# Kernel optimization log

Measured on AMD Instinct MI355X. Metric: run time of the kernel, lower is better.

The kernel has to match this reference:

```python
import jax, jax.numpy as jnp
import numpy as np
from jax import lax

RANK = 8
ALPHA = 16.0
SCALING = ALPHA / RANK  # 2.0
C_IN, C_OUT, KH, KW = 128, 256, 3, 3


def setup_inputs() -> dict:
    key = jax.random.key(0)
    k1, k2, k3, k4, k5 = jax.random.split(key, 5)
    x = jax.random.normal(k1, (16, C_IN, 64, 64), dtype=jnp.float32)
    W = jax.random.normal(k2, (C_OUT, C_IN, KH, KW), dtype=jnp.float32) * 0.05
    b = jax.random.normal(k3, (C_OUT,), dtype=jnp.float32) * 0.05
    lora_A = jax.random.normal(k4, (RANK, C_IN * KH * KW), dtype=jnp.float32) * 0.02
    lora_B = jax.random.normal(k5, (C_OUT, RANK), dtype=jnp.float32) * 0.02
    return {"x": x, "W": W, "b": b, "lora_A": lora_A, "lora_B": lora_B}


def _conv(x, w, stride=(1, 1), padding=((1, 1), (1, 1))):
    return lax.conv_general_dilated(
        x, w, window_strides=stride, padding=padding,
        dimension_numbers=("NCHW", "OIHW", "NCHW"))


def reference(x, W, b, lora_A, lora_B):
    # Base (frozen) conv: [B, C_out, H, W]
    base_out = _conv(x, W) + b[None, :, None, None]
    # LoRA path. The torch code does im2col -> (BL, C_in*kh*kw) @ A.T @ B.T.
    # Because unfold flattens patches channel-major as (C_in, kh, kw), the
    # identical math is: rank-r conv with A reshaped as [rank, C_in, kh, kw],
    # then a 1x1 mix with B. Same result, no im2col materialization.
    A_k = lora_A.reshape(RANK, C_IN, KH, KW)
    h = _conv(x, A_k)                                   # [B, rank, H, W]
    lora_out = jnp.einsum("brhw,or->bohw", h, lora_B) * SCALING
    return base_out + lora_out
```

## Files before the change

kernel.cpp:

```cpp
#include <hip/hip_runtime.h>
#include <hip/hip_bf16.h>


#define CIN   128
#define COUT  256
#define NBAT  16
#define HPAD  66
#define WPAD  66

typedef __bf16 bf16x8 __attribute__((ext_vector_type(8)));
typedef float f32x4 __attribute__((ext_vector_type(4)));

#define XPAD_ELEMS ((size_t)NBAT * HPAD * WPAD * CIN)
#define XPAD_BYTES (XPAD_ELEMS * 2)
#define WT_ELEMS   ((size_t)9 * COUT * CIN)
#define WS_NEED    (XPAD_BYTES + WT_ELEMS * 2)

typedef __attribute__((address_space(1))) void gvoid;
typedef __attribute__((address_space(3))) void lvoid;

__device__ __forceinline__ void load_lds16(const void* g, void* l) {
    __builtin_amdgcn_global_load_lds((gvoid*)g, (lvoid*)l, 16, 0, 0);
}

__global__ void pad_prep(const float* __restrict__ x, __bf16* __restrict__ xpad,
                         const float* __restrict__ W, const float* __restrict__ lA,
                         const float* __restrict__ lB, __hip_bfloat16* __restrict__ Wt) {
    __shared__ float tile[128][66];
    const int t = threadIdx.x;

    if (blockIdx.x >= 1024) {
        const int idx = (blockIdx.x - 1024) * 256 + t;
        const int c = idx & 127;
        const int o = idx >> 7;
        float lb[8];
#pragma unroll
        for (int r = 0; r < 8; ++r) lb[r] = lB[o * 8 + r];
#pragma unroll
        for (int tap = 0; tap < 9; ++tap) {
            float acc = W[(o * 128 + c) * 9 + tap];
            float s = 0.f;
#pragma unroll
            for (int r = 0; r < 8; ++r)
                s += lb[r] * lA[r * 1152 + c * 9 + tap];
            Wt[tap * 32768 + idx] = __float2bfloat16(acc + 2.0f * s);
        }
        return;
    }

    const int n = blockIdx.x >> 6;
    const int h = blockIdx.x & 63;
    const float* src = x + (size_t)n * 128 * 4096 + (size_t)h * 64;
#pragma unroll
    for (int i = 0; i < 8; ++i) {
        int g  = i * 256 + t;
        int c  = g >> 4;
        int w4 = (g & 15) * 4;
        const float4 v = *reinterpret_cast<const float4*>(src + (size_t)c * 4096 + w4);
        const int wb = w4 ^ (((c >> 3) & 7) << 2);
        tile[c][wb + 0] = v.x; tile[c][wb + 1] = v.y;
        tile[c][wb + 2] = v.z; tile[c][wb + 3] = v.w;
    }
    __syncthreads();
    __bf16* dst = xpad + ((size_t)(n * 66 + h + 1) * 66 + 1) * 128;
#pragma unroll
    for (int i = 0; i < 4; ++i) {
        int g  = i * 256 + t;
        int w  = g >> 4;
        int c0 = (g & 15) * 8;
        const int swr = ((c0 >> 3) & 7) << 2;
        bf16x8 v;
#pragma unroll
        for (int j = 0; j < 8; ++j) v[j] = (__bf16)tile[c0 + j][w ^ swr];
        *reinterpret_cast<bf16x8*>(dst + (size_t)w * 128 + c0) = v;
    }
    bf16x8 z = {};
    __bf16* rowbase = xpad + (size_t)(n * 66 + h + 1) * 66 * 128;
    if (t < 32) {
        int ww = (t < 16) ? 0 : 65;
        int c0 = (t & 15) * 8;
        *reinterpret_cast<bf16x8*>(rowbase + (size_t)ww * 128 + c0) = z;
    }
    if (h == 0 || h == 63) {
        __bf16* hrow = xpad + (size_t)(n * 66 + (h == 0 ? 0 : 65)) * 66 * 128;
        for (int i = t; i < 66 * 16; i += 256)
            *reinterpret_cast<bf16x8*>(hrow + (size_t)i * 8) = z;
    }
}

__global__ void __launch_bounds__(512, 2) conv_mfma(
    const __bf16* __restrict__ xpad, const __bf16* __restrict__ Wt,
    const float* __restrict__ bias, float* __restrict__ out) {
    __shared__ __align__(16) __bf16 lds[65536];

    const int tid  = threadIdx.x;
    const int wv   = tid >> 6;
    const int lane = tid & 63;

    const int n  = blockIdx.x >> 4;
    const int h0 = (blockIdx.x & 15) << 2;

    const int lrow = lane >> 2;
    const int lswz = (((lane & 3) ^ (lrow & 3)) << 3);
    const __bf16* aG[2];
    const __bf16* bG[2];
#pragma unroll
    for (int j = 0; j < 2; ++j) {
        const int r0 = j * 128 + wv * 16;
        aG[j] = Wt + (r0 + lrow) * 128 + lswz;
        bG[j] = xpad + (((size_t)(n * 66 + h0 + (r0 >> 6)) * 66 + (r0 & 63) + lrow) * 128) + lswz;
    }

    const int wo   = (wv >> 2) << 7;
    const int wpix = (wv & 3) << 6;
    const int fr   = lane & 15;
    const int fphys = (((lane >> 4) ^ (lane & 3)) << 3);
    const int a_rd = (wo + fr) * 32 + fphys;
    const int b_rd = (wpix + fr) * 32 + fphys;

    f32x4 acc[8][4] = {};

#define STAGE(u) do {                                                          \
        const int tap_ = (u) >> 2, cb_ = (u) & 3;                              \
        const int kh_ = (tap_ >= 6) ? 2 : (tap_ >= 3 ? 1 : 0);                 \
        const int kw_ = tap_ - kh_ * 3;                                        \
        const int ao_ = tap_ * 32768 + cb_ * 32;                               \
        const int bo_ = (kh_ * 66 + kw_) * 128 + cb_ * 32;                     \
        const int lb_ = ((u) & 3) * 8192;                                      \
        load_lds16(aG[0] + ao_, lds + lb_ + (wv * 16) * 32);                   \
        load_lds16(aG[1] + ao_, lds + lb_ + (128 + wv * 16) * 32);             \
        load_lds16(bG[0] + bo_, lds + 32768 + lb_ + (wv * 16) * 32);           \
        load_lds16(bG[1] + bo_, lds + 32768 + lb_ + (128 + wv * 16) * 32);     \
    } while (0)

#define COMPUTE(t) do {                                                        \
        const int lb_ = ((t) & 3) * 8192;                                      \
        const __bf16* Ab = lds + lb_ + a_rd;                                   \
        const __bf16* Bb = lds + 32768 + lb_ + b_rd;                           \
        bf16x8 af[8], bfr[4];                                                  \
        _Pragma("unroll")                                                      \
        for (int ni = 0; ni < 4; ++ni)                                         \
            bfr[ni] = *reinterpret_cast<const bf16x8*>(Bb + ni * 512);         \
        _Pragma("unroll")                                                      \
        for (int mi = 0; mi < 8; ++mi)                                         \
            af[mi] = *reinterpret_cast<const bf16x8*>(Ab + mi * 512);          \
        __builtin_amdgcn_s_setprio(1);                                         \
        _Pragma("unroll")                                                      \
        for (int mi = 0; mi < 8; ++mi)                                         \
            _Pragma("unroll")                                                  \
            for (int ni = 0; ni < 4; ++ni)                                     \
                acc[mi][ni] = __builtin_amdgcn_mfma_f32_16x16x32_bf16(         \
                    af[mi], bfr[ni], acc[mi][ni], 0, 0, 0);                    \
        __builtin_amdgcn_s_setprio(0);                                         \
    } while (0)

    STAGE(0); STAGE(1); STAGE(2);

    for (int t = 0; t < 33; ++t) {
        asm volatile("s_waitcnt vmcnt(8)" ::: "memory");
        __builtin_amdgcn_sched_barrier(0);
        __builtin_amdgcn_s_barrier();
        __builtin_amdgcn_sched_barrier(0);
        STAGE(t + 3);
        COMPUTE(t);
    }
    asm volatile("s_waitcnt vmcnt(8)" ::: "memory");
    __builtin_amdgcn_sched_barrier(0);
    __builtin_amdgcn_s_barrier();
    COMPUTE(33);
    asm volatile("s_waitcnt vmcnt(4)" ::: "memory");
    __builtin_amdgcn_sched_barrier(0);
    __builtin_amdgcn_s_barrier();
    COMPUTE(34);
    asm volatile("s_waitcnt vmcnt(0)" ::: "memory");
    __builtin_amdgcn_sched_barrier(0);
    __builtin_amdgcn_s_barrier();
    COMPUTE(35);

#undef STAGE
#undef COMPUTE

    const int col  = lane & 15;
    const int orow = (lane >> 4) << 2;
    const int h    = h0 + (wpix >> 6);
#pragma unroll
    for (int mi = 0; mi < 8; ++mi) {
        const int obm = wo + mi * 16 + orow;
#pragma unroll
        for (int j = 0; j < 4; ++j) {
            const int o = obm + j;
            const float bj = bias[o];
            float* orow_ptr = out + (((size_t)n * 256 + o) * 64 + h) * 64;
#pragma unroll
            for (int ni = 0; ni < 4; ++ni)
                orow_ptr[ni * 16 + col] = acc[mi][ni][j] + bj;
        }
    }
}

__global__ void conv_naive(const float* __restrict__ x, const float* __restrict__ W,
                           const float* __restrict__ b, const float* __restrict__ lA,
                           const float* __restrict__ lB, float* __restrict__ out) {
    int idx = blockIdx.x * 256 + threadIdx.x;
    int w = idx & 63, h = (idx >> 6) & 63, o = (idx >> 12) & 255, n = idx >> 20;
    float acc = b[o];
    float hr[8] = {0, 0, 0, 0, 0, 0, 0, 0};
    for (int c = 0; c < 128; ++c)
        for (int kh = 0; kh < 3; ++kh) {
            int hy = h + kh - 1;
            if (hy < 0 || hy > 63) continue;
            for (int kw = 0; kw < 3; ++kw) {
                int wx = w + kw - 1;
                if (wx < 0 || wx > 63) continue;
                float xv = x[((n * 128 + c) * 64 + hy) * 64 + wx];
                int ka = c * 9 + kh * 3 + kw;
                acc += W[(o * 128 + c) * 9 + kh * 3 + kw] * xv;
#pragma unroll
                for (int r = 0; r < 8; ++r) hr[r] += lA[r * 1152 + ka] * xv;
            }
        }
    float ls = 0.f;
#pragma unroll
    for (int r = 0; r < 8; ++r) ls += lB[o * 8 + r] * hr[r];
    out[idx] = acc + 2.0f * ls;
}

extern "C" void kernel_launch(void* const* d_in, const int* in_sizes, int n_in,
                              void* d_out, int out_size, void* d_ws, size_t ws_size,
                              hipStream_t stream) {
    const float* x  = (const float*)d_in[0];
    const float* W  = (const float*)d_in[1];
    const float* b  = (const float*)d_in[2];
    const float* lA = (const float*)d_in[3];
    const float* lB = (const float*)d_in[4];
    float* out = (float*)d_out;

    if (ws_size < WS_NEED) {
        conv_naive<<<out_size / 256, 256, 0, stream>>>(x, W, b, lA, lB, out);
        return;
    }

    __bf16* xpad = (__bf16*)d_ws;
    __hip_bfloat16* Wt = (__hip_bfloat16*)((char*)d_ws + XPAD_BYTES);

    pad_prep<<<1024 + 128, 256, 0, stream>>>(x, xpad, W, lA, lB, Wt);
    conv_mfma<<<256, 512, 0, stream>>>(xpad, (const __bf16*)Wt, b, out);
}
```

Measured before the change: 134.5 us.

## Swap MFMA operand order for vectorized output stores and adjust LDS swizzle

Swaps the MFMA operands so the accumulator holds four consecutive output pixels per lane instead of four output channels. The epilogue can then write 16-byte float4 stores along the width dimension instead of scattered scalar stores. It also changes the LDS XOR swizzle used for global-to-LDS loads and fragment reads, presumably to cut bank conflicts. The swizzle change must match on the write and read sides, or the results will be wrong.

```diff
diff --git a/kernel.cpp b/kernel.cpp
--- a/kernel.cpp
+++ b/kernel.cpp
@@ -101,7 +101,7 @@
     const int h0 = (blockIdx.x & 15) << 2;
 
     const int lrow = lane >> 2;
-    const int lswz = (((lane & 3) ^ (lrow & 3)) << 3);
+    const int lswz = (((lane & 3) ^ ((lane >> 3) & 3)) << 3);
     const __bf16* aG[2];
     const __bf16* bG[2];
 #pragma unroll
@@ -114,11 +114,11 @@
     const int wo   = (wv >> 2) << 7;
     const int wpix = (wv & 3) << 6;
     const int fr   = lane & 15;
-    const int fphys = (((lane >> 4) ^ (lane & 3)) << 3);
+    const int fphys = (((lane >> 4) ^ ((lane >> 1) & 3)) << 3);
     const int a_rd = (wo + fr) * 32 + fphys;
     const int b_rd = (wpix + fr) * 32 + fphys;
 
-    f32x4 acc[8][4] = {};
+    f32x4 acc[4][8] = {};
 
 #define STAGE(u) do {                                                          \
         const int tap_ = (u) >> 2, cb_ = (u) & 3;                              \
@@ -139,18 +139,18 @@
         const __bf16* Bb = lds + 32768 + lb_ + b_rd;                           \
         bf16x8 af[8], bfr[4];                                                  \
         _Pragma("unroll")                                                      \
-        for (int ni = 0; ni < 4; ++ni)                                         \
-            bfr[ni] = *reinterpret_cast<const bf16x8*>(Bb + ni * 512);         \
+        for (int pi = 0; pi < 4; ++pi)                                         \
+            bfr[pi] = *reinterpret_cast<const bf16x8*>(Bb + pi * 512);         \
         _Pragma("unroll")                                                      \
-        for (int mi = 0; mi < 8; ++mi)                                         \
-            af[mi] = *reinterpret_cast<const bf16x8*>(Ab + mi * 512);          \
+        for (int oi = 0; oi < 8; ++oi)                                         \
+            af[oi] = *reinterpret_cast<const bf16x8*>(Ab + oi * 512);          \
         __builtin_amdgcn_s_setprio(1);                                         \
         _Pragma("unroll")                                                      \
-        for (int mi = 0; mi < 8; ++mi)                                         \
+        for (int pi = 0; pi < 4; ++pi)                                         \
             _Pragma("unroll")                                                  \
-            for (int ni = 0; ni < 4; ++ni)                                     \
-                acc[mi][ni] = __builtin_amdgcn_mfma_f32_16x16x32_bf16(         \
-                    af[mi], bfr[ni], acc[mi][ni], 0, 0, 0);                    \
+            for (int oi = 0; oi < 8; ++oi)                                     \
+                acc[pi][oi] = __builtin_amdgcn_mfma_f32_16x16x32_bf16(         \
+                    bfr[pi], af[oi], acc[pi][oi], 0, 0, 0);                    \
         __builtin_amdgcn_s_setprio(0);                                         \
     } while (0)
 
@@ -180,20 +180,22 @@
 #undef STAGE
 #undef COMPUTE
 
-    const int col  = lane & 15;
-    const int orow = (lane >> 4) << 2;
-    const int h    = h0 + (wpix >> 6);
-#pragma unroll
-    for (int mi = 0; mi < 8; ++mi) {
-        const int obm = wo + mi * 16 + orow;
-#pragma unroll
-        for (int j = 0; j < 4; ++j) {
-            const int o = obm + j;
-            const float bj = bias[o];
-            float* orow_ptr = out + (((size_t)n * 256 + o) * 64 + h) * 64;
-#pragma unroll
-            for (int ni = 0; ni < 4; ++ni)
-                orow_ptr[ni * 16 + col] = acc[mi][ni][j] + bj;
+    const int col = lane & 15;
+    const int q4  = (lane >> 4) << 2;
+    const int h   = h0 + (wpix >> 6);
+    float bo[8];
+#pragma unroll
+    for (int oi = 0; oi < 8; ++oi) bo[oi] = bias[wo + oi * 16 + col];
+#pragma unroll
+    for (int pi = 0; pi < 4; ++pi) {
+        const int w0 = pi * 16 + q4;
+#pragma unroll
+        for (int oi = 0; oi < 8; ++oi) {
+            const int o = wo + oi * 16 + col;
+            f32x4 v;
+#pragma unroll
+            for (int j = 0; j < 4; ++j) v[j] = acc[pi][oi][j] + bo[oi];
+            *reinterpret_cast<f32x4*>(out + (((size_t)n * 256 + o) * 64 + h) * 64 + w0) = v;
         }
     }
 }
```

Result: no change. 137.0 us (+1.8%).
